# Kernel optimization log

Hardware: AMD Instinct MI355X
Metric: run time of the kernel (lower is better)

The kernel has to match this reference:

```python
import jax, jax.numpy as jnp
import numpy as np

B, D, C, L, H, HF, HG, NCLS = 4096, 2048, 16, 128, 256, 512, 128, 200

def _init(key, shape, fan_in):
    return jax.random.normal(key, shape, dtype=jnp.float32) * (1.0 / np.sqrt(fan_in))

def setup_inputs() -> dict:
    key = jax.random.key(0)
    ks = jax.random.split(key, 16)
    return {
        "x": jax.random.normal(ks[0], (B, D), dtype=jnp.float32),
        "fp": jax.random.uniform(ks[1], (C, D), minval=-1.0, maxval=1.0, dtype=jnp.float32),  # probability_vector_logits
        "mean_inputs": jax.random.normal(ks[2], (D,), dtype=jnp.float32) * 0.1,
        "Wg1": _init(ks[3], (C, D, H), D), "bg1": jnp.zeros((C, H), jnp.float32),
        "Wg2": _init(ks[4], (C, H, L), H), "bg2": jnp.zeros((C, L), jnp.float32),
        "Wf1": _init(ks[5], (D, HF), D), "bf1": jnp.zeros((HF,), jnp.float32),
        "Wf2": _init(ks[6], (HF, L), HF), "bf2": jnp.zeros((L,), jnp.float32),
        "Wg_head": _init(ks[7], (C * (L // 2), HG), C * (L // 2)), "bg_head": jnp.zeros((HG,), jnp.float32),
        "Wc": _init(ks[8], (HG, NCLS), HG), "bc": jnp.zeros((NCLS,), jnp.float32),
    }

def _l2_normalize(v, axis):
    # tf.math.l2_normalize: v * rsqrt(max(sum(v^2), 1e-12))
    sq = jnp.sum(v * v, axis=axis, keepdims=True)
    return v * jax.lax.rsqrt(jnp.maximum(sq, 1e-12))

def reference(x, fp, mean_inputs, Wg1, bg1, Wg2, bg2, Wf1, bf1, Wf2, bf2, Wg_head, bg_head, Wc, bc):
    # Deterministic forward (training=False, forward_deterministic=True)
    gate = jax.nn.sigmoid(fp)  # [C, D]
    # mask_features: gate*x + (1-gate)*mean, vectorized over concepts -> [C, B, D]
    masked = gate[:, None, :] * x[None, :, :] + (1.0 - gate)[:, None, :] * mean_inputs[None, None, :]
    # per-concept generator MLPs (distinct weights per concept) -> concept_matrix [B, C, L]
    h = jax.nn.relu(jnp.einsum('cbd,cdh->cbh', masked, Wg1) + bg1[:, None, :])
    cm = jnp.einsum('cbh,chl->cbl', h, Wg2) + bg2[:, None, :]
    cm = jnp.transpose(cm, (1, 0, 2))              # [B, C, L]
    cm_norm = _l2_normalize(cm, axis=1)            # normalize across concept axis (axis=1 in TF code)
    # shared features_to_concepts model applied to each masked_x -> latent [C, B, L]
    hf = jax.nn.relu(jnp.einsum('cbd,dh->cbh', masked, Wf1) + bf1)
    latent = jnp.einsum('cbh,hl->cbl', hf, Wf2) + bf2
    latent = jnp.transpose(latent, (1, 0, 2))      # [B, C, L]
    # concept scores: sigmoid(<cm_norm[b,c,:], latent[b,c,:]>)
    concept_prob = jax.nn.sigmoid(jnp.sum(cm_norm * latent, axis=-1))  # [B, C]
    half = L // 2
    p = concept_prob[:, :, None]
    bottleneck = p * cm_norm[:, :, half:] + (1.0 - p) * cm_norm[:, :, :half]  # [B, C, L/2]
    bottleneck = bottleneck.reshape(bottleneck.shape[0], -1)                   # [B, C*L/2]
    # g_model + concepts_to_labels head
    z = jax.nn.relu(bottleneck @ Wg_head + bg_head)
    logits = z @ Wc + bc  # [B, NCLS]
    return logits
```

## Files before the change

kernel.cpp:

```cpp
#include <hip/hip_runtime.h>
#include <hip/hip_bf16.h>

typedef __bf16 bf16;
typedef __attribute__((ext_vector_type(8))) __bf16 bf16x8;
typedef __attribute__((ext_vector_type(4))) float f32x4;

__device__ __forceinline__ void gload_lds16(const void* g, void* l) {
    __builtin_amdgcn_global_load_lds(
        (const __attribute__((address_space(1))) unsigned int*)g,
        (__attribute__((address_space(3))) unsigned int*)l, 16, 0, 0);
}

#define BARRIER()   asm volatile("s_barrier" ::: "memory")
#define WAITLGKM0() asm volatile("s_waitcnt lgkmcnt(0)" ::: "memory")
#define WAITVM4()   asm volatile("s_waitcnt vmcnt(4)" ::: "memory")
#define WAITVM0()   asm volatile("s_waitcnt vmcnt(0)" ::: "memory")
#define SCHED0()    __builtin_amdgcn_sched_barrier(0)


__global__ void cvt_x(const float* __restrict__ in, bf16* __restrict__ out) {
    const long i = ((long)blockIdx.x * 256 + threadIdx.x) * 8;
    float4 v0 = *(const float4*)(in + i);
    float4 v1 = *(const float4*)(in + i + 4);
    bf16x8 o;
    o[0]=(bf16)v0.x; o[1]=(bf16)v0.y; o[2]=(bf16)v0.z; o[3]=(bf16)v0.w;
    o[4]=(bf16)v1.x; o[5]=(bf16)v1.y; o[6]=(bf16)v1.z; o[7]=(bf16)v1.w;
    *(bf16x8*)(out + i) = o;
}

template <int SCALED>
__global__ void prep_w(const float* __restrict__ in, bf16* __restrict__ out,
                       int R, int S, long in_bstride, long out_bstride,
                       const float* __restrict__ fp, const float* __restrict__ mean,
                       float* __restrict__ corr)
{
    __shared__ float tile[32][33];
    const int s0 = blockIdx.x * 32, r0 = blockIdx.y * 32;
    const int tx = threadIdx.x & 31, ty = threadIdx.x >> 5;
    const int batch = blockIdx.z;
    const float* inb = in + (long)batch * in_bstride;
#pragma unroll
    for (int i = 0; i < 32; i += 8)
        tile[ty + i][tx] = inb[(long)(r0 + ty + i) * S + s0 + tx];
    __syncthreads();
    bf16* outb = out + (long)batch * out_bstride;
    float gv = 1.f, gmv = 0.f;
    if (SCALED) {
        gv = 1.f / (1.f + expf(-fp[(long)batch * R + r0 + tx]));
        gmv = (1.f - gv) * mean[r0 + tx];
    }
#pragma unroll
    for (int i = 0; i < 32; i += 8) {
        const float wv = tile[tx][ty + i];
        outb[(long)(s0 + ty + i) * R + r0 + tx] = (bf16)(gv * wv);
        if (SCALED) {
            float v = gmv * wv;
#pragma unroll
            for (int off = 16; off; off >>= 1) v += __shfl_xor(v, off);
            if (tx == 0) atomicAdd(&corr[(long)batch * S + s0 + ty + i], v);
        }
    }
}

__global__ void prep_small(const float* __restrict__ Wg2, bf16* __restrict__ Wg2T,
                           const float* __restrict__ Wf2, bf16* __restrict__ Wf2T,
                           const float* __restrict__ Wgh, bf16* __restrict__ WghT)
{
    __shared__ float tile[32][33];
    const int b = blockIdx.x;
    const float* in; bf16* out; int R, bx, by;
    if (b < 512) {
        const int z = b >> 5, rem = b & 31;
        bx = rem & 3; by = rem >> 2; R = 256;
        in = Wg2 + (long)z * 256 * 128; out = Wg2T + (long)z * 128 * 256;
    } else if (b < 576) {
        const int rem = b - 512;
        bx = rem & 3; by = rem >> 2; R = 512;
        in = Wf2; out = Wf2T;
    } else {
        const int rem = b - 576;
        bx = rem & 3; by = rem >> 2; R = 1024;
        in = Wgh; out = WghT;
    }
    const int s0 = bx * 32, r0 = by * 32;
    const int tx = threadIdx.x & 31, ty = threadIdx.x >> 5;
#pragma unroll
    for (int i = 0; i < 32; i += 8)
        tile[ty + i][tx] = in[(long)(r0 + ty + i) * 128 + s0 + tx];
    __syncthreads();
#pragma unroll
    for (int i = 0; i < 32; i += 8)
        out[(long)(s0 + ty + i) * R + r0 + tx] = (bf16)tile[tx][ty + i];
}

__global__ __launch_bounds__(512, 2)
void gemm256(const bf16* __restrict__ A, const bf16* __restrict__ Wall,
             const float* __restrict__ bg1, const float* __restrict__ corr_g,
             const float* __restrict__ bf1, const float* __restrict__ corr_f,
             bf16* __restrict__ h_out, bf16* __restrict__ hf_out)
{
    __shared__ __align__(16) bf16 lds[2][4][8192];

    const int bid = blockIdx.x;
    const int swz = (bid & 7) * 96 + (bid >> 3);
    const int c   = swz / 48;
    const int rem = swz % 48;
    const int ny  = rem / 16;
    const int m0  = (rem % 16) * 256;

    const int t = threadIdx.x, lane = t & 63, w = t >> 6;
    const int wr = w >> 2, wc = w & 3;
    const bf16* Bc = Wall + (long)c * 768 * 2048;

    const int rr = lane >> 3;
    const int qq = (lane & 7) ^ rr;
    const bf16* pA0 = A  + (long)(m0 + w * 16 + rr) * 2048 + qq * 8;
    const bf16* pA1 = pA0 + 8 * 2048;
    const bf16* pB0 = Bc + (long)(ny * 256 + w * 16 + rr) * 2048 + qq * 8;
    const bf16* pB1 = pB0 + 8 * 2048;

    const int l15 = lane & 15;
    const int q0 = (((lane >> 4) ^ (lane & 7))) * 8;
    const int aoff0 = l15 * 64 + q0, aoff1 = aoff0 ^ 32;
    const int boff0 = ((wc & 1) * 64 + l15) * 64 + q0, boff1 = boff0 ^ 32;
    const int hb = 2 + (wc >> 1);

    f32x4 acc[8][4] = {};
    bf16x8 Ax[4][2], Ay[4][2], Bx[2][2], By[2][2];

#define STG(buf, half, P0, P1, e) do { \
    gload_lds16((P0) + (e), &lds[buf][half][w * 1024]); \
    gload_lds16((P1) + (e), &lds[buf][half][w * 1024 + 512]); } while (0)

#define RDA(dst, buf, mb) do { _Pragma("unroll") \
    for (int mm = 0; mm < 4; ++mm) { \
        dst[mm][0] = *(const bf16x8*)&lds[buf][wr][aoff0 + (mb + mm) * 1024]; \
        dst[mm][1] = *(const bf16x8*)&lds[buf][wr][aoff1 + (mb + mm) * 1024]; } } while (0)

#define RDB(dst, buf, nh) do { _Pragma("unroll") \
    for (int nn = 0; nn < 2; ++nn) { \
        dst[nn][0] = *(const bf16x8*)&lds[buf][hb][boff0 + (nh * 2 + nn) * 1024]; \
        dst[nn][1] = *(const bf16x8*)&lds[buf][hb][boff1 + (nh * 2 + nn) * 1024]; } } while (0)

#define MFMA16(mb, Af, Bf, nh) do { __builtin_amdgcn_s_setprio(1); _Pragma("unroll") \
    for (int kk = 0; kk < 2; ++kk) { _Pragma("unroll") \
      for (int mm = 0; mm < 4; ++mm) { _Pragma("unroll") \
        for (int nn = 0; nn < 2; ++nn) { \
            acc[mb + mm][nh * 2 + nn] = __builtin_amdgcn_mfma_f32_16x16x32_bf16( \
                Af[mm][kk], Bf[nn][kk], acc[mb + mm][nh * 2 + nn], 0, 0, 0); } } } \
    __builtin_amdgcn_s_setprio(0); } while (0)

    STG(0, 0, pA0, pA1, 0);
    STG(0, 1, pA0, pA1, 262144);
    STG(0, 2, pB0, pB1, 0);
    STG(0, 3, pB0, pB1, 262144);
    STG(1, 2, pB0, pB1, 64);
    STG(1, 3, pB0, pB1, 262144 + 64);
    WAITVM4();
    BARRIER();
    RDA(Ax, 0, 0); RDB(Bx, 0, 0);

#pragma unroll 1
    for (int it = 0; it < 16; ++it) {
        const int kB  = (2 * it + 1) * 64;
        const int kA2 = ((2 * it + 2) & 31) * 64;
        const int kB2 = ((2 * it + 3) & 31) * 64;
        STG(1, 0, pA0, pA1, kB);
        BARRIER();
        RDB(By, 0, 1);
        SCHED0();
        MFMA16(0, Ax, Bx, 0);
        BARRIER();
        STG(1, 1, pA0, pA1, 262144 + kB);
        BARRIER();
        RDA(Ay, 0, 4);
        SCHED0();
        MFMA16(0, Ax, By, 1);
        BARRIER();
        STG(0, 2, pB0, pB1, kA2);
        BARRIER();
        MFMA16(4, Ay, By, 1);
        BARRIER();
        STG(0, 3, pB0, pB1, 262144 + kA2);
        WAITVM4();
        BARRIER();
        RDA(Ax, 1, 0);
        SCHED0();
        MFMA16(4, Ay, Bx, 0);
        RDB(Bx, 1, 0);
        BARRIER();
        STG(0, 0, pA0, pA1, kA2);
        BARRIER();
        RDB(By, 1, 1);
        SCHED0();
        MFMA16(0, Ax, Bx, 0);
        BARRIER();
        STG(0, 1, pA0, pA1, 262144 + kA2);
        BARRIER();
        RDA(Ay, 1, 4);
        SCHED0();
        MFMA16(0, Ax, By, 1);
        BARRIER();
        STG(1, 2, pB0, pB1, kB2);
        BARRIER();
        MFMA16(4, Ay, By, 1);
        BARRIER();
        STG(1, 3, pB0, pB1, 262144 + kB2);
        WAITVM4();
        BARRIER();
        RDA(Ax, 0, 0);
        SCHED0();
        MFMA16(4, Ay, Bx, 0);
        RDB(Bx, 0, 0);
        BARRIER();
    }

    WAITVM0(); WAITLGKM0();
    BARRIER();
    bf16* cst = (bf16*)&lds[0][0][0];
    const int r4 = (lane >> 4) * 4;
    const int isH = (ny == 0);
    const int N = isH ? 256 : 512;
#pragma unroll
    for (int n = 0; n < 4; ++n) {
        const int cl = wc * 64 + n * 16 + l15;
        float bv;
        if (isH) bv = bg1[c * 256 + cl] + corr_g[c * 256 + cl];
        else {
            const int cf = (ny - 1) * 256 + cl;
            bv = bf1[cf] + corr_f[c * 512 + cf];
        }
#pragma unroll
        for (int m = 0; m < 8; ++m)
#pragma unroll
            for (int j = 0; j < 4; ++j) {
                const int row = wr * 128 + m * 16 + r4 + j;
                cst[row * 256 + cl] = (bf16)fmaxf(acc[m][n][j] + bv, 0.0f);
            }
    }
    BARRIER();
    bf16* obase = isH ? h_out + ((long)c * 4096 + m0) * 256
                      : hf_out + ((long)c * 4096 + m0) * 512 + (ny - 1) * 256;
    const int trow = t >> 5, tch = (t & 31) * 8;
#pragma unroll
    for (int pass = 0; pass < 16; ++pass) {
        const int row = pass * 16 + trow;
        *(bf16x8*)&obase[(long)row * N + tch] = *(const bf16x8*)&cst[row * 256 + tch];
    }
#undef STG
#undef RDA
#undef RDB
#undef MFMA16
}

template <int RELU, int HASBIAS, int OUTBF>
__global__ __launch_bounds__(256, 2)
void gemm_bf16_kernel(const bf16* __restrict__ A, const bf16* __restrict__ Wt,
                      const float* __restrict__ bias, void* __restrict__ outv,
                      int Kloop, int lda, int ldb,
                      long a_zoff, long w_zoff, long b_cstride,
                      long out_rstride, long out_zoff)
{
    __shared__ __align__(16) bf16 As[128 * 64];
    __shared__ __align__(16) bf16 Bs[128 * 64];

    const int z  = blockIdx.z;
    const int m0 = blockIdx.x * 128;
    const int n0 = blockIdx.y * 128;
    const int t  = threadIdx.x;
    const int lane = t & 63, wave = t >> 6;
    const int wr = wave >> 1, wc = wave & 1;

    const bf16* Ac = A  + (long)z * a_zoff;
    const bf16* W  = Wt + (long)z * w_zoff;
    const long obase = (long)z * out_zoff + (long)m0 * out_rstride + n0;

    const int sr = t >> 3;
    const int sc = (t & 7) * 8;

    f32x4 acc[4][4] = {};

    for (int kt = 0; kt < Kloop / 64; ++kt) {
        const int k0 = kt * 64;
#pragma unroll
        for (int i = 0; i < 4; ++i)
            gload_lds16(Ac + (long)(m0 + i * 32 + sr) * lda + k0 + sc, &As[i * 2048 + wave * 512]);
#pragma unroll
        for (int i = 0; i < 4; ++i)
            gload_lds16(W + (long)(n0 + i * 32 + sr) * ldb + k0 + sc, &Bs[i * 2048 + wave * 512]);
        __syncthreads();

#pragma unroll
        for (int kk = 0; kk < 2; ++kk) {
            bf16x8 af[4], bfr[4];
#pragma unroll
            for (int m = 0; m < 4; ++m)
                af[m] = *(const bf16x8*)&As[(wr * 64 + m * 16 + (lane & 15)) * 64 + kk * 32 + (lane >> 4) * 8];
#pragma unroll
            for (int n = 0; n < 4; ++n)
                bfr[n] = *(const bf16x8*)&Bs[(wc * 64 + n * 16 + (lane & 15)) * 64 + kk * 32 + (lane >> 4) * 8];
#pragma unroll
            for (int m = 0; m < 4; ++m)
#pragma unroll
                for (int n = 0; n < 4; ++n)
                    acc[m][n] = __builtin_amdgcn_mfma_f32_16x16x32_bf16(af[m], bfr[n], acc[m][n], 0, 0, 0);
        }
        __syncthreads();
    }

    const int ci = lane & 15, r4 = (lane >> 4) * 4;
#pragma unroll
    for (int m = 0; m < 4; ++m)
#pragma unroll
        for (int n = 0; n < 4; ++n) {
            const int col = wc * 64 + n * 16 + ci;
            float bv = 0.f;
            if (HASBIAS) bv = bias[(long)z * b_cstride + n0 + col];
#pragma unroll
            for (int j = 0; j < 4; ++j) {
                const int row = wr * 64 + m * 16 + r4 + j;
                float v = acc[m][n][j] + bv;
                if (RELU) v = fmaxf(v, 0.0f);
                const long idx = obase + (long)row * out_rstride + col;
                if (OUTBF) ((bf16*)outv)[idx] = (bf16)v;
                else       ((float*)outv)[idx] = v;
            }
        }
}

__global__ void fuse_kernel(const bf16* __restrict__ cm, const bf16* __restrict__ lat,
                            bf16* __restrict__ bott)
{
    const int wave = threadIdx.x >> 6;
    const int l    = threadIdx.x & 63;
    const int b    = blockIdx.x * 4 + wave;
    const bf16* cmb = cm  + (size_t)b * 2048;
    const bf16* lb  = lat + (size_t)b * 2048;

    float vc0[16], vc1[16], vl0[16], vl1[16];
    float sq0 = 0.f, sq1 = 0.f;
#pragma unroll
    for (int c = 0; c < 16; ++c) {
        float c0 = (float)cmb[c * 128 + l], c1 = (float)cmb[c * 128 + 64 + l];
        vc0[c] = c0; vc1[c] = c1;
        vl0[c] = (float)lb[c * 128 + l];
        vl1[c] = (float)lb[c * 128 + 64 + l];
        sq0 += c0 * c0; sq1 += c1 * c1;
    }
    const float rs0 = rsqrtf(fmaxf(sq0, 1e-12f));
    const float rs1 = rsqrtf(fmaxf(sq1, 1e-12f));
#pragma unroll
    for (int c = 0; c < 16; ++c) {
        const float cn0 = vc0[c] * rs0, cn1 = vc1[c] * rs1;
        float part = cn0 * vl0[c] + cn1 * vl1[c];
#pragma unroll
        for (int off = 32; off; off >>= 1) part += __shfl_xor(part, off);
        const float p = 1.0f / (1.0f + expf(-part));
        bott[(size_t)b * 1024 + c * 64 + l] = (bf16)(p * cn1 + (1.0f - p) * cn0);
    }
}

__global__ void head2_kernel(const float* __restrict__ zp, const float* __restrict__ bgh,
                             const float* __restrict__ Wc, const float* __restrict__ bc,
                             float* __restrict__ out)
{
    __shared__ float zs[8][128];
    const int b0 = blockIdx.x * 8;
    const int t = threadIdx.x;
#pragma unroll
    for (int i = 0; i < 4; ++i) {
        const int idx = t + i * 256;
        const int r = idx >> 7, k = idx & 127;
        float s = bgh[k];
#pragma unroll
        for (int ks = 0; ks < 8; ++ks) s += zp[(size_t)ks * 524288 + (size_t)(b0 + r) * 128 + k];
        zs[r][k] = fmaxf(s, 0.0f);
    }
    __syncthreads();
    if (t < 200) {
        float a[8];
#pragma unroll
        for (int r = 0; r < 8; ++r) a[r] = bc[t];
        for (int k = 0; k < 128; ++k) {
            const float wv = Wc[k * 200 + t];
#pragma unroll
            for (int r = 0; r < 8; ++r) a[r] = fmaf(zs[r][k], wv, a[r]);
        }
#pragma unroll
        for (int r = 0; r < 8; ++r) out[(size_t)(b0 + r) * 200 + t] = a[r];
    }
}


extern "C" void kernel_launch(void* const* d_in, const int* in_sizes, int n_in,
                              void* d_out, int out_size, void* d_ws, size_t ws_size,
                              hipStream_t stream)
{
    (void)in_sizes; (void)n_in; (void)out_size; (void)ws_size;

    const float* x    = (const float*)d_in[0];
    const float* fp   = (const float*)d_in[1];
    const float* mean = (const float*)d_in[2];
    const float* Wg1  = (const float*)d_in[3];
    const float* bg1  = (const float*)d_in[4];
    const float* Wg2  = (const float*)d_in[5];
    const float* bg2  = (const float*)d_in[6];
    const float* Wf1  = (const float*)d_in[7];
    const float* bf1  = (const float*)d_in[8];
    const float* Wf2  = (const float*)d_in[9];
    const float* bf2  = (const float*)d_in[10];
    const float* Wgh  = (const float*)d_in[11];
    const float* bgh  = (const float*)d_in[12];
    const float* Wc   = (const float*)d_in[13];
    const float* bc   = (const float*)d_in[14];
    float* outp = (float*)d_out;

    char* p = (char*)d_ws;
    size_t off = 0;
    auto alloc = [&](size_t bytes) { void* r = p + off; off += (bytes + 255) & ~(size_t)255; return r; };
    bf16*  xbf    = (bf16*) alloc((size_t)4096 * 2048 * 2);
    bf16*  Wall   = (bf16*) alloc((size_t)16 * 768 * 2048 * 2);
    bf16*  Wg2T   = (bf16*) alloc((size_t)16 * 128 * 256 * 2);
    bf16*  Wf2T   = (bf16*) alloc((size_t)128 * 512 * 2);
    bf16*  WghT   = (bf16*) alloc((size_t)128 * 1024 * 2);
    float* corr_g = (float*)alloc((size_t)16 * 256 * 4);
    float* corr_f = (float*)alloc((size_t)16 * 512 * 4);
    bf16*  h      = (bf16*) alloc((size_t)16 * 4096 * 256 * 2);
    bf16*  hf     = (bf16*) alloc((size_t)16 * 4096 * 512 * 2);
    bf16*  cm     = (bf16*) alloc((size_t)4096 * 2048 * 2);
    bf16*  lat    = (bf16*) alloc((size_t)4096 * 2048 * 2);
    bf16*  bott   = (bf16*) alloc((size_t)4096 * 1024 * 2);
    float* zp     = (float*)alloc((size_t)8 * 4096 * 128 * 4);

    hipMemsetAsync(corr_g, 0, (size_t)(16 * 256 + 16 * 512) * 4, stream);
    cvt_x<<<4096, 256, 0, stream>>>(x, xbf);

    prep_w<1><<<dim3(8, 64, 16), 256, 0, stream>>>(
        Wg1, Wall, 2048, 256, (long)2048 * 256, (long)768 * 2048, fp, mean, corr_g);
    prep_w<1><<<dim3(16, 64, 16), 256, 0, stream>>>(
        Wf1, Wall + (size_t)256 * 2048, 2048, 512, 0, (long)768 * 2048, fp, mean, corr_f);
    prep_small<<<704, 256, 0, stream>>>(Wg2, Wg2T, Wf2, Wf2T, Wgh, WghT);

    gemm256<<<768, 512, 0, stream>>>(xbf, Wall, bg1, corr_g, bf1, corr_f, h, hf);

    gemm_bf16_kernel<0, 1, 1><<<dim3(32, 1, 16), 256, 0, stream>>>(
        h, Wg2T, bg2, cm, 256, 256, 256, (long)4096 * 256, (long)128 * 256, 128, 2048, 128);
    gemm_bf16_kernel<0, 1, 1><<<dim3(32, 1, 16), 256, 0, stream>>>(
        hf, Wf2T, bf2, lat, 512, 512, 512, (long)4096 * 512, 0, 0, 2048, 128);

    fuse_kernel<<<1024, 256, 0, stream>>>(cm, lat, bott);

    gemm_bf16_kernel<0, 0, 0><<<dim3(32, 1, 8), 256, 0, stream>>>(
        bott, WghT, nullptr, zp, 128, 1024, 1024, 128, 128, 0, 128, (long)4096 * 128);

    head2_kernel<<<512, 256, 0, stream>>>(zp, bgh, Wc, bc, outp);
}
```

Baseline: 383.4 us.

## Merge prep and mid GEMM launches, drop atomics, peel gemm256 tail, vectorize fuse

The two weight-prep launches become one combined transpose kernel, and the gate-mean correction is now computed by separate dot-product kernels instead of per-element atomics, which also removes the memset. The two second-layer GEMMs share a single launch, and the head GEMM gets a specialized kernel. The main gemm256 loop peels its last iteration so it no longer issues wasted wraparound prefetches. The fuse kernel reads packed bf16 pairs and writes packed output. The aim is fewer launches, no atomic contention and less redundant memory traffic, at the cost of extra small kernels that re-read the fp32 weights for the correction.

```diff
diff --git a/kernel.cpp b/kernel.cpp
--- a/kernel.cpp
+++ b/kernel.cpp
@@ -16,6 +16,13 @@
 #define WAITVM4()   asm volatile("s_waitcnt vmcnt(4)" ::: "memory")
 #define WAITVM0()   asm volatile("s_waitcnt vmcnt(0)" ::: "memory")
 #define SCHED0()    __builtin_amdgcn_sched_barrier(0)
+
+__device__ __forceinline__ unsigned int pack2(float a, float b) {
+    bf16 x = (bf16)a, y = (bf16)b;
+    unsigned short ux, uy;
+    __builtin_memcpy(&ux, &x, 2); __builtin_memcpy(&uy, &y, 2);
+    return (unsigned int)ux | ((unsigned int)uy << 16);
+}
 
 
 __global__ void cvt_x(const float* __restrict__ in, bf16* __restrict__ out) {
@@ -28,38 +35,54 @@
     *(bf16x8*)(out + i) = o;
 }
 
-template <int SCALED>
-__global__ void prep_w(const float* __restrict__ in, bf16* __restrict__ out,
-                       int R, int S, long in_bstride, long out_bstride,
-                       const float* __restrict__ fp, const float* __restrict__ mean,
-                       float* __restrict__ corr)
+__global__ void prep_gmv(const float* __restrict__ fp, const float* __restrict__ mean,
+                         float* __restrict__ gmv) {
+    const int i = blockIdx.x * 256 + threadIdx.x;
+    const float g = 1.f / (1.f + expf(-fp[i]));
+    gmv[i] = (1.f - g) * mean[i & 2047];
+}
+
+template <int SHARED_W>
+__global__ void corr_kernel(const float* __restrict__ W, const float* __restrict__ gmv,
+                            float* __restrict__ corr, int S) {
+    __shared__ float red[4][64];
+    const int c = blockIdx.y;
+    const int sl = threadIdx.x & 63;
+    const int s = blockIdx.x * 64 + sl;
+    const int w = threadIdx.x >> 6;
+    const float* Wc = W + (SHARED_W ? 0 : (long)c * 2048 * S);
+    const float* gm = gmv + c * 2048;
+    float acc = 0.f;
+#pragma unroll 4
+    for (int r = w; r < 2048; r += 4)
+        acc = fmaf(gm[r], Wc[(long)r * S + s], acc);
+    red[w][sl] = acc;
+    __syncthreads();
+    if (w == 0)
+        corr[(long)c * S + s] = red[0][sl] + red[1][sl] + red[2][sl] + red[3][sl];
+}
+
+__global__ void prep_big(const float* __restrict__ Wg1, const float* __restrict__ Wf1,
+                         bf16* __restrict__ Wall, const float* __restrict__ fp)
 {
     __shared__ float tile[32][33];
-    const int s0 = blockIdx.x * 32, r0 = blockIdx.y * 32;
+    const int z = blockIdx.z;
+    const int bx = blockIdx.x;
+    const int r0 = blockIdx.y * 32;
     const int tx = threadIdx.x & 31, ty = threadIdx.x >> 5;
-    const int batch = blockIdx.z;
-    const float* inb = in + (long)batch * in_bstride;
+    const float* in; bf16* out; int S, s0;
+    if (bx < 8) { S = 256; s0 = bx * 32; in = Wg1 + (long)z * 2048 * 256;
+                  out = Wall + (long)z * 768 * 2048; }
+    else        { S = 512; s0 = (bx - 8) * 32; in = Wf1;
+                  out = Wall + (long)z * 768 * 2048 + (long)256 * 2048; }
 #pragma unroll
     for (int i = 0; i < 32; i += 8)
-        tile[ty + i][tx] = inb[(long)(r0 + ty + i) * S + s0 + tx];
+        tile[ty + i][tx] = in[(long)(r0 + ty + i) * S + s0 + tx];
     __syncthreads();
-    bf16* outb = out + (long)batch * out_bstride;
-    float gv = 1.f, gmv = 0.f;
-    if (SCALED) {
-        gv = 1.f / (1.f + expf(-fp[(long)batch * R + r0 + tx]));
-        gmv = (1.f - gv) * mean[r0 + tx];
-    }
-#pragma unroll
-    for (int i = 0; i < 32; i += 8) {
-        const float wv = tile[tx][ty + i];
-        outb[(long)(s0 + ty + i) * R + r0 + tx] = (bf16)(gv * wv);
-        if (SCALED) {
-            float v = gmv * wv;
-#pragma unroll
-            for (int off = 16; off; off >>= 1) v += __shfl_xor(v, off);
-            if (tx == 0) atomicAdd(&corr[(long)batch * S + s0 + ty + i], v);
-        }
-    }
+    const float gv = 1.f / (1.f + expf(-fp[z * 2048 + r0 + tx]));
+#pragma unroll
+    for (int i = 0; i < 32; i += 8)
+        out[(long)(s0 + ty + i) * 2048 + r0 + tx] = (bf16)(gv * tile[tx][ty + i]);
 }
 
 __global__ void prep_small(const float* __restrict__ Wg2, bf16* __restrict__ Wg2T,
@@ -161,10 +184,10 @@
     RDA(Ax, 0, 0); RDB(Bx, 0, 0);
 
 #pragma unroll 1
-    for (int it = 0; it < 16; ++it) {
+    for (int it = 0; it < 15; ++it) {
         const int kB  = (2 * it + 1) * 64;
-        const int kA2 = ((2 * it + 2) & 31) * 64;
-        const int kB2 = ((2 * it + 3) & 31) * 64;
+        const int kA2 = (2 * it + 2) * 64;
+        const int kB2 = (2 * it + 3) * 64;
         STG(1, 0, pA0, pA1, kB);
         BARRIER();
         RDB(By, 0, 1);
@@ -215,7 +238,42 @@
         BARRIER();
     }
 
-    WAITVM0(); WAITLGKM0();
+    {
+        const int kB = 31 * 64;
+        STG(1, 0, pA0, pA1, kB);
+        BARRIER();
+        RDB(By, 0, 1);
+        SCHED0();
+        MFMA16(0, Ax, Bx, 0);
+        BARRIER();
+        STG(1, 1, pA0, pA1, 262144 + kB);
+        BARRIER();
+        RDA(Ay, 0, 4);
+        SCHED0();
+        MFMA16(0, Ax, By, 1);
+        BARRIER();
+        MFMA16(4, Ay, By, 1);
+        BARRIER();
+        WAITVM0();
+        BARRIER();
+        RDA(Ax, 1, 0);
+        SCHED0();
+        MFMA16(4, Ay, Bx, 0);
+        RDB(Bx, 1, 0);
+        BARRIER();
+        RDB(By, 1, 1);
+        SCHED0();
+        MFMA16(0, Ax, Bx, 0);
+        BARRIER();
+        RDA(Ay, 1, 4);
+        SCHED0();
+        MFMA16(0, Ax, By, 1);
+        BARRIER();
+        MFMA16(4, Ay, By, 1);
+        MFMA16(4, Ay, Bx, 0);
+    }
+
+    WAITLGKM0();
     BARRIER();
     bf16* cst = (bf16*)&lds[0][0][0];
     const int r4 = (lane >> 4) * 4;
@@ -253,41 +311,44 @@
 #undef MFMA16
 }
 
-template <int RELU, int HASBIAS, int OUTBF>
 __global__ __launch_bounds__(256, 2)
-void gemm_bf16_kernel(const bf16* __restrict__ A, const bf16* __restrict__ Wt,
-                      const float* __restrict__ bias, void* __restrict__ outv,
-                      int Kloop, int lda, int ldb,
-                      long a_zoff, long w_zoff, long b_cstride,
-                      long out_rstride, long out_zoff)
+void gemm_mid(const bf16* __restrict__ h, const bf16* __restrict__ hf,
+              const bf16* __restrict__ Wg2T, const bf16* __restrict__ Wf2T,
+              const float* __restrict__ bg2, const float* __restrict__ bf2,
+              bf16* __restrict__ cm, bf16* __restrict__ lat)
 {
     __shared__ __align__(16) bf16 As[128 * 64];
     __shared__ __align__(16) bf16 Bs[128 * 64];
 
     const int z  = blockIdx.z;
     const int m0 = blockIdx.x * 128;
-    const int n0 = blockIdx.y * 128;
     const int t  = threadIdx.x;
     const int lane = t & 63, wave = t >> 6;
     const int wr = wave >> 1, wc = wave & 1;
 
-    const bf16* Ac = A  + (long)z * a_zoff;
-    const bf16* W  = Wt + (long)z * w_zoff;
-    const long obase = (long)z * out_zoff + (long)m0 * out_rstride + n0;
+    int K; const bf16 *Ac, *W; const float* bias; bf16* outp;
+    if (z < 16) {
+        K = 256; Ac = h + (long)z * 4096 * 256; W = Wg2T + (long)z * 128 * 256;
+        bias = bg2 + z * 128; outp = cm + (long)m0 * 2048 + z * 128;
+    } else {
+        const int c = z - 16;
+        K = 512; Ac = hf + (long)c * 4096 * 512; W = Wf2T;
+        bias = bf2; outp = lat + (long)m0 * 2048 + c * 128;
+    }
 
     const int sr = t >> 3;
     const int sc = (t & 7) * 8;
 
     f32x4 acc[4][4] = {};
 
-    for (int kt = 0; kt < Kloop / 64; ++kt) {
+    for (int kt = 0; kt < K / 64; ++kt) {
         const int k0 = kt * 64;
 #pragma unroll
         for (int i = 0; i < 4; ++i)
-            gload_lds16(Ac + (long)(m0 + i * 32 + sr) * lda + k0 + sc, &As[i * 2048 + wave * 512]);
+            gload_lds16(Ac + (long)(m0 + i * 32 + sr) * K + k0 + sc, &As[i * 2048 + wave * 512]);
 #pragma unroll
         for (int i = 0; i < 4; ++i)
-            gload_lds16(W + (long)(n0 + i * 32 + sr) * ldb + k0 + sc, &Bs[i * 2048 + wave * 512]);
+            gload_lds16(W + (long)(i * 32 + sr) * K + k0 + sc, &Bs[i * 2048 + wave * 512]);
         __syncthreads();
 
 #pragma unroll
@@ -314,49 +375,112 @@
 #pragma unroll
         for (int n = 0; n < 4; ++n) {
             const int col = wc * 64 + n * 16 + ci;
-            float bv = 0.f;
-            if (HASBIAS) bv = bias[(long)z * b_cstride + n0 + col];
+            const float bv = bias[col];
 #pragma unroll
             for (int j = 0; j < 4; ++j) {
                 const int row = wr * 64 + m * 16 + r4 + j;
-                float v = acc[m][n][j] + bv;
-                if (RELU) v = fmaxf(v, 0.0f);
-                const long idx = obase + (long)row * out_rstride + col;
-                if (OUTBF) ((bf16*)outv)[idx] = (bf16)v;
-                else       ((float*)outv)[idx] = v;
+                outp[(long)row * 2048 + col] = (bf16)(acc[m][n][j] + bv);
             }
         }
 }
 
-__global__ void fuse_kernel(const bf16* __restrict__ cm, const bf16* __restrict__ lat,
-                            bf16* __restrict__ bott)
+__global__ __launch_bounds__(256, 2)
+void gemm_zp(const bf16* __restrict__ A, const bf16* __restrict__ Wt,
+             float* __restrict__ outf)
+{
+    __shared__ __align__(16) bf16 As[128 * 64];
+    __shared__ __align__(16) bf16 Bs[128 * 64];
+
+    const int z  = blockIdx.z;
+    const int m0 = blockIdx.x * 128;
+    const int t  = threadIdx.x;
+    const int lane = t & 63, wave = t >> 6;
+    const int wr = wave >> 1, wc = wave & 1;
+
+    const bf16* Ac = A  + (long)z * 128;
+    const bf16* W  = Wt + (long)z * 128;
+    float* outp = outf + (long)z * 4096 * 128 + (long)m0 * 128;
+
+    const int sr = t >> 3;
+    const int sc = (t & 7) * 8;
+
+    f32x4 acc[4][4] = {};
+
+    for (int kt = 0; kt < 2; ++kt) {
+        const int k0 = kt * 64;
+#pragma unroll
+        for (int i = 0; i < 4; ++i)
+            gload_lds16(Ac + (long)(m0 + i * 32 + sr) * 1024 + k0 + sc, &As[i * 2048 + wave * 512]);
+#pragma unroll
+        for (int i = 0; i < 4; ++i)
+            gload_lds16(W + (long)(i * 32 + sr) * 1024 + k0 + sc, &Bs[i * 2048 + wave * 512]);
+        __syncthreads();
+
+#pragma unroll
+        for (int kk = 0; kk < 2; ++kk) {
+            bf16x8 af[4], bfr[4];
+#pragma unroll
+            for (int m = 0; m < 4; ++m)
+                af[m] = *(const bf16x8*)&As[(wr * 64 + m * 16 + (lane & 15)) * 64 + kk * 32 + (lane >> 4) * 8];
+#pragma unroll
+            for (int n = 0; n < 4; ++n)
+                bfr[n] = *(const bf16x8*)&Bs[(wc * 64 + n * 16 + (lane & 15)) * 64 + kk * 32 + (lane >> 4) * 8];
+#pragma unroll
+            for (int m = 0; m < 4; ++m)
+#pragma unroll
+                for (int n = 0; n < 4; ++n)
+                    acc[m][n] = __builtin_amdgcn_mfma_f32_16x16x32_bf16(af[m], bfr[n], acc[m][n], 0, 0, 0);
+        }
+        __syncthreads();
+    }
+
+    const int ci = lane & 15, r4 = (lane >> 4) * 4;
+#pragma unroll
+    for (int m = 0; m < 4; ++m)
+#pragma unroll
+        for (int n = 0; n < 4; ++n) {
+            const int col = wc * 64 + n * 16 + ci;
+#pragma unroll
+            for (int j = 0; j < 4; ++j) {
+                const int row = wr * 64 + m * 16 + r4 + j;
+                outp[(long)row * 128 + col] = acc[m][n][j];
+            }
+        }
+}
+
+__global__ void fuse_kernel(const unsigned int* __restrict__ cm, const unsigned int* __restrict__ lat,
+                            unsigned int* __restrict__ bott)
 {
     const int wave = threadIdx.x >> 6;
     const int l    = threadIdx.x & 63;
     const int b    = blockIdx.x * 4 + wave;
-    const bf16* cmb = cm  + (size_t)b * 2048;
-    const bf16* lb  = lat + (size_t)b * 2048;
-
-    float vc0[16], vc1[16], vl0[16], vl1[16];
+    const unsigned int* cu = cm  + (size_t)b * 1024;
+    const unsigned int* lu = lat + (size_t)b * 1024;
+
+    float c0[16], c1[16], l0[16], l1[16];
     float sq0 = 0.f, sq1 = 0.f;
 #pragma unroll
     for (int c = 0; c < 16; ++c) {
-        float c0 = (float)cmb[c * 128 + l], c1 = (float)cmb[c * 128 + 64 + l];
-        vc0[c] = c0; vc1[c] = c1;
-        vl0[c] = (float)lb[c * 128 + l];
-        vl1[c] = (float)lb[c * 128 + 64 + l];
-        sq0 += c0 * c0; sq1 += c1 * c1;
+        const unsigned int vc = cu[c * 64 + l], vl = lu[c * 64 + l];
+        c0[c] = __uint_as_float(vc << 16);
+        c1[c] = __uint_as_float(vc & 0xffff0000u);
+        l0[c] = __uint_as_float(vl << 16);
+        l1[c] = __uint_as_float(vl & 0xffff0000u);
+        sq0 += c0[c] * c0[c]; sq1 += c1[c] * c1[c];
     }
     const float rs0 = rsqrtf(fmaxf(sq0, 1e-12f));
     const float rs1 = rsqrtf(fmaxf(sq1, 1e-12f));
 #pragma unroll
     for (int c = 0; c < 16; ++c) {
-        const float cn0 = vc0[c] * rs0, cn1 = vc1[c] * rs1;
-        float part = cn0 * vl0[c] + cn1 * vl1[c];
+        const float cn0 = c0[c] * rs0, cn1 = c1[c] * rs1;
+        float part = cn0 * l0[c] + cn1 * l1[c];
 #pragma unroll
         for (int off = 32; off; off >>= 1) part += __shfl_xor(part, off);
         const float p = 1.0f / (1.0f + expf(-part));
-        bott[(size_t)b * 1024 + c * 64 + l] = (bf16)(p * cn1 + (1.0f - p) * cn0);
+        const float o0 = __shfl_xor(cn0, 32), o1 = __shfl_xor(cn1, 32);
+        if (l < 32)
+            bott[(size_t)b * 512 + c * 32 + l] =
+                pack2(p * o0 + (1.f - p) * cn0, p * o1 + (1.f - p) * cn1);
     }
 }
 
@@ -423,6 +547,7 @@
     bf16*  Wg2T   = (bf16*) alloc((size_t)16 * 128 * 256 * 2);
     bf16*  Wf2T   = (bf16*) alloc((size_t)128 * 512 * 2);
     bf16*  WghT   = (bf16*) alloc((size_t)128 * 1024 * 2);
+    float* gmv    = (float*)alloc((size_t)16 * 2048 * 4);
     float* corr_g = (float*)alloc((size_t)16 * 256 * 4);
     float* corr_f = (float*)alloc((size_t)16 * 512 * 4);
     bf16*  h      = (bf16*) alloc((size_t)16 * 4096 * 256 * 2);
@@ -432,26 +557,21 @@
     bf16*  bott   = (bf16*) alloc((size_t)4096 * 1024 * 2);
     float* zp     = (float*)alloc((size_t)8 * 4096 * 128 * 4);
 
-    hipMemsetAsync(corr_g, 0, (size_t)(16 * 256 + 16 * 512) * 4, stream);
     cvt_x<<<4096, 256, 0, stream>>>(x, xbf);
-
-    prep_w<1><<<dim3(8, 64, 16), 256, 0, stream>>>(
-        Wg1, Wall, 2048, 256, (long)2048 * 256, (long)768 * 2048, fp, mean, corr_g);
-    prep_w<1><<<dim3(16, 64, 16), 256, 0, stream>>>(
-        Wf1, Wall + (size_t)256 * 2048, 2048, 512, 0, (long)768 * 2048, fp, mean, corr_f);
+    prep_gmv<<<128, 256, 0, stream>>>(fp, mean, gmv);
+    prep_big<<<dim3(24, 64, 16), 256, 0, stream>>>(Wg1, Wf1, Wall, fp);
     prep_small<<<704, 256, 0, stream>>>(Wg2, Wg2T, Wf2, Wf2T, Wgh, WghT);
+    corr_kernel<0><<<dim3(4, 16), 256, 0, stream>>>(Wg1, gmv, corr_g, 256);
+    corr_kernel<1><<<dim3(8, 16), 256, 0, stream>>>(Wf1, gmv, corr_f, 512);
 
     gemm256<<<768, 512, 0, stream>>>(xbf, Wall, bg1, corr_g, bf1, corr_f, h, hf);
 
-    gemm_bf16_kernel<0, 1, 1><<<dim3(32, 1, 16), 256, 0, stream>>>(
-        h, Wg2T, bg2, cm, 256, 256, 256, (long)4096 * 256, (long)128 * 256, 128, 2048, 128);
-    gemm_bf16_kernel<0, 1, 1><<<dim3(32, 1, 16), 256, 0, stream>>>(
-        hf, Wf2T, bf2, lat, 512, 512, 512, (long)4096 * 512, 0, 0, 2048, 128);
-
-    fuse_kernel<<<1024, 256, 0, stream>>>(cm, lat, bott);
-
-    gemm_bf16_kernel<0, 0, 0><<<dim3(32, 1, 8), 256, 0, stream>>>(
-        bott, WghT, nullptr, zp, 128, 1024, 1024, 128, 128, 0, 128, (long)4096 * 128);
+    gemm_mid<<<dim3(32, 1, 32), 256, 0, stream>>>(h, hf, Wg2T, Wf2T, bg2, bf2, cm, lat);
+
+    fuse_kernel<<<1024, 256, 0, stream>>>((const unsigned int*)cm, (const unsigned int*)lat,
+                                          (unsigned int*)bott);
+
+    gemm_zp<<<dim3(32, 1, 8), 256, 0, stream>>>(bott, WghT, zp);
 
     head2_kernel<<<512, 256, 0, stream>>>(zp, bgh, Wc, bc, outp);
 }
```

Result: faster. 362.8 us (-5.4%).
